# Performance work log

Measured on AMD Instinct MI355X. Metric: run time of the kernel, lower is better.

## Reference

```python
import jax, jax.numpy as jnp
import numpy as np

NUM_LEAVES = 8192
N_LAMBDA = 2101  # wavelengths 400..2500 nm

# ---- exponential integral E1(x), x > 0 (Abramowitz & Stegun 5.1.53 / 5.1.56) ----
# Ei(-x) = -E1(x) for x > 0; forward only ever calls expi on -kall with kall >= 1e-4.
_A = jnp.array([-0.57721566, 0.99999193, -0.24991055, 0.05519968, -0.00976004, 0.00107857], dtype=jnp.float32)
_PN = jnp.array([1.0, 8.5733287401, 18.0590169730, 8.6347608925, 0.2677737343], dtype=jnp.float32)
_PD = jnp.array([1.0, 9.5733223454, 25.6329561486, 21.0996530827, 3.9584969228], dtype=jnp.float32)

def _poly(c, x):
    r = c[0]
    for ci in c[1:]:
        r = r * x + ci
    return r

def _e1(x):
    # x > 0 guaranteed (kall clamped to >= 1e-4)
    small = -jnp.log(x) + _poly(_A[::-1], x)          # 0 < x <= 1
    big = jnp.exp(-x) / x * (_poly(_PN, x) / _poly(_PD, x))  # x > 1
    return jnp.where(x <= 1.0, small, big)

# ---- transmissivity of a dielectric plane (Stern / Allen) ----
def _getav(alpha_deg, nr):
    n2 = nr ** 2
    npx = n2 + 1.0
    nm = n2 - 1.0
    a = (nr + 1.0) * (nr + 1.0) / 2.0
    k = -(n2 - 1.0) * (n2 - 1.0) / 4.0
    rd = alpha_deg * (np.pi / 180.0)
    sa2 = np.sin(rd) ** 2  # python scalar
    if alpha_deg != 90.0:
        b1 = jnp.sqrt((sa2 - npx / 2.0) ** 2 + k)
    else:
        b1 = 0.0
    b2 = sa2 - npx / 2.0
    b = b1 - b2
    k2 = k ** 2
    ts = k2 / (6.0 * b ** 3) + k / b - b / 2.0 - (k2 / (6.0 * a ** 3) + k / a - a / 2.0)
    tp1 = -2.0 * n2 * (b - a) / npx ** 2
    nm2 = nm ** 2
    tp2 = -2.0 * n2 * npx * jnp.log(b / a) / nm2
    tp3 = n2 * (1.0 / b - 1.0 / a) / 2.0
    n22 = n2 ** 2
    npx3 = npx ** 3
    npax_a = 2.0 * npx * a - nm2
    npx_b = 2.0 * npx * b - nm2
    tp4 = 16.0 * n22 * (n22 + 1.0) * jnp.log(npx_b / npax_a) / (npx3 * nm2)
    tp5 = 16.0 * n2 ** 3 * (1.0 / npx_b - 1.0 / npax_a) / npx3
    tp = tp1 + tp2 + tp3 + tp4 + tp5
    return (ts + tp) / (2.0 * sa2)

def _forward(N, cab, car, water, lma, cant, nr, kab, kcar, kant, kw, km):
    # kall: [L, W] via broadcasting of [L,1] traits against [W] spectra
    kall = (cab * kab + car * kcar + cant * kant + water * kw + lma * km) / N
    kall = jnp.maximum(kall, 1e-4)
    # tau = (1-k)e^{-k} + k^2 * (-Ei(-k)) = (1-k)e^{-k} + k^2 E1(k)
    tau = (1.0 - kall) * jnp.exp(-kall) + kall ** 2 * _e1(kall)

    # one-layer reflectance/transmittance
    talf = _getav(40.0, nr)
    ralf = 1.0 - talf
    t12 = _getav(90.0, nr)
    r12 = 1.0 - t12
    t21 = t12 / (nr * nr)
    r21 = 1.0 - t21
    denom = 1.0 - r21 * r21 * tau * tau
    Ta = talf * tau * t21 / denom
    Ra = ralf + r21 * tau * Ta
    t = t12 * tau * t21 / denom
    r = r12 + r21 * tau * t

    rpt = r + t
    rmt = r - t
    mask = rpt >= 1.0  # [L, W]
    Dsq = (1.0 + rpt) * (1.0 + rmt) * (1.0 - rmt) * (1.0 - rpt)
    D = jnp.sqrt(jnp.where(mask, 1.0, Dsq))
    rqmtq = r ** 2 - t ** 2
    a = (1.0 + rqmtq + D) / (2.0 * r)
    b = (1.0 - rqmtq + D) / (2.0 * t)
    b_safe = jnp.where(mask, 1.0, b)  # guard pow with float exponent
    bnm1 = b_safe ** (N - 1.0)
    bn2 = bnm1 ** 2
    a2 = a * a
    den2 = a2 * bn2 - 1.0
    Rsub = a * (bn2 - 1.0) / den2
    Tsub = bnm1 * (a2 - 1.0) / den2
    # thick-layer (r+t >= 1) limit
    Tsub_alt = t / (t + (1.0 - t) * (N - 1.0))
    Tsub = jnp.where(mask, Tsub_alt, Tsub)
    Rsub = jnp.where(mask, 1.0 - Tsub_alt, Rsub)

    den3 = 1.0 - Rsub * r
    tran = Ta * Tsub / den3
    refl = Ra + Ta_Rsub_term(Ta, Rsub, t, den3)
    return refl, tran

def Ta_Rsub_term(Ta, Rsub, t, den3):
    return Ta * Rsub * t / den3

def setup_inputs() -> dict:
    key = jax.random.key(0)
    ks = jax.random.split(key, 12)
    u = lambda k, shp: jax.random.uniform(k, shp, dtype=jnp.float32)
    L, W = NUM_LEAVES, N_LAMBDA
    return {
        "N":     1.0 + 1.5 * u(ks[0], (L, 1)),      # leaf structure 1..2.5
        "cab":   10.0 + 70.0 * u(ks[1], (L, 1)),    # chlorophyll ug/cm2
        "car":   2.0 + 18.0 * u(ks[2], (L, 1)),     # carotenoids
        "water": 0.002 + 0.03 * u(ks[3], (L, 1)),   # EWT cm
        "lma":   0.005 + 0.03 * u(ks[4], (L, 1)),   # dry matter g/cm2
        "cant":  2.0 * u(ks[5], (L, 1)),            # anthocyanins
        "nr":    1.3 + 0.3 * u(ks[6], (W,)),        # refractive index
        "kab":   0.05 * u(ks[7], (W,)),
        "kcar":  0.05 * u(ks[8], (W,)),
        "kant":  0.05 * u(ks[9], (W,)),
        "kw":    30.0 * u(ks[10], (W,)),
        "km":    60.0 * u(ks[11], (W,)),
    }

def reference(N, cab, car, water, lma, cant, nr, kab, kcar, kant, kw, km):
    return _forward(N, cab, car, water, lma, cant, nr, kab, kcar, kant, kw, km)
```

## Files before the change

kernel.cpp:

```cpp
#include <hip/hip_runtime.h>

#define L_LEAVES 8192
#define W_LAMBDA 2101
#define WPAD     2104
#define SA2_40   0.41317591116653485f
#define LOG2E_F  1.4426950408889634f
#define LN2_F    0.6931471805599453f

__device__ __forceinline__ float rcpf(float x)  { return __builtin_amdgcn_rcpf(x); }
__device__ __forceinline__ float log2f_fast(float x) { return __builtin_amdgcn_logf(x); }
__device__ __forceinline__ float exp2f_fast(float x) { return __builtin_amdgcn_exp2f(x); }
__device__ __forceinline__ float sqrtf_fast(float x) { return __builtin_amdgcn_sqrtf(x); }

__device__ __forceinline__ float getav_dev(float sa2, bool is90, float nr) {
    float n2  = nr * nr;
    float npx = n2 + 1.0f;
    float nm  = n2 - 1.0f;
    float a   = (nr + 1.0f) * (nr + 1.0f) * 0.5f;
    float k   = -(n2 - 1.0f) * (n2 - 1.0f) * 0.25f;
    float b2  = sa2 - npx * 0.5f;
    float b1  = is90 ? 0.0f : sqrtf(b2 * b2 + k);
    float b   = b1 - b2;
    float k2  = k * k;
    float b3  = b * b * b;
    float a3  = a * a * a;
    float ts  = k2 / (6.0f * b3) + k / b - b * 0.5f
              - (k2 / (6.0f * a3) + k / a - a * 0.5f);
    float tp1 = -2.0f * n2 * (b - a) / (npx * npx);
    float nm2 = nm * nm;
    float tp2 = -2.0f * n2 * npx * logf(b / a) / nm2;
    float tp3 = n2 * (1.0f / b - 1.0f / a) * 0.5f;
    float n22 = n2 * n2;
    float npx3 = npx * npx * npx;
    float npax_a = 2.0f * npx * a - nm2;
    float npx_b  = 2.0f * npx * b - nm2;
    float tp4 = 16.0f * n22 * (n22 + 1.0f) * logf(npx_b / npax_a) / (npx3 * nm2);
    float tp5 = 16.0f * n2 * n2 * n2 * (1.0f / npx_b - 1.0f / npax_a) / npx3;
    float tp  = tp1 + tp2 + tp3 + tp4 + tp5;
    return (ts + tp) / (2.0f * sa2);
}

__global__ void precompute_kernel(const float* __restrict__ nr, float* __restrict__ tab) {
    int w = blockIdx.x * blockDim.x + threadIdx.x;
    if (w >= W_LAMBDA) return;
    float n    = nr[w];
    float talf = getav_dev(SA2_40, false, n);
    float t12  = getav_dev(1.0f,   true,  n);
    float t21  = t12 * rcpf(n * n);
    float r21  = 1.0f - t21;
    tab[0 * WPAD + w] = talf * t21;
    tab[1 * WPAD + w] = 1.0f - talf;
    tab[2 * WPAD + w] = t12 * t21;
    tab[3 * WPAD + w] = 1.0f - t12;
    tab[4 * WPAD + w] = r21;
    tab[5 * WPAD + w] = r21 * r21;
}

struct f4u { float v[4]; };

__device__ __forceinline__ float vget(const float4& v, int j) {
    return j == 0 ? v.x : (j == 1 ? v.y : (j == 2 ? v.z : v.w));
}

template<bool USE_TAB>
__global__ __launch_bounds__(192) void prospect_kernel(
    const float* __restrict__ pN,   const float* __restrict__ pcab,
    const float* __restrict__ pcar, const float* __restrict__ pwater,
    const float* __restrict__ plma, const float* __restrict__ pcant,
    const float* __restrict__ pnr,
    const float* __restrict__ pkab, const float* __restrict__ pkcar,
    const float* __restrict__ pkant, const float* __restrict__ pkw,
    const float* __restrict__ pkm,
    const float* __restrict__ tab,
    float* __restrict__ out)
{
    const int q  = blockIdx.x * blockDim.x + threadIdx.x;
    const int w0 = q * 4;
    if (w0 >= W_LAMBDA) return;
    const bool full = (w0 + 4 <= W_LAMBDA);

    const int l = blockIdx.y;
    const float Nl   = pN[l];
    const float invN = rcpf(Nl);
    const float Nm1  = Nl - 1.0f;
    const float cabl = pcab[l], carl = pcar[l], cantl = pcant[l];
    const float watl = pwater[l], lmal = plma[l];
    const size_t LW = (size_t)L_LEAVES * W_LAMBDA;

    float4 vkab, vkcar, vkant, vkw, vkm;
    float4 t0, t1, t2, t3, t4, t5;
    if (full) {
        vkab  = *(const float4*)(pkab  + w0);
        vkcar = *(const float4*)(pkcar + w0);
        vkant = *(const float4*)(pkant + w0);
        vkw   = *(const float4*)(pkw   + w0);
        vkm   = *(const float4*)(pkm   + w0);
        if (USE_TAB) {
            t0 = *(const float4*)(tab + 0 * WPAD + w0);
            t1 = *(const float4*)(tab + 1 * WPAD + w0);
            t2 = *(const float4*)(tab + 2 * WPAD + w0);
            t3 = *(const float4*)(tab + 3 * WPAD + w0);
            t4 = *(const float4*)(tab + 4 * WPAD + w0);
            t5 = *(const float4*)(tab + 5 * WPAD + w0);
        }
    } else {
        float* a[5] = {nullptr};
        #pragma unroll
        for (int j = 0; j < 4; ++j) {
            int w = min(w0 + j, W_LAMBDA - 1);
            ((float*)&vkab)[j]  = pkab[w];
            ((float*)&vkcar)[j] = pkcar[w];
            ((float*)&vkant)[j] = pkant[w];
            ((float*)&vkw)[j]   = pkw[w];
            ((float*)&vkm)[j]   = pkm[w];
            if (USE_TAB) {
                ((float*)&t0)[j] = tab[0 * WPAD + w];
                ((float*)&t1)[j] = tab[1 * WPAD + w];
                ((float*)&t2)[j] = tab[2 * WPAD + w];
                ((float*)&t3)[j] = tab[3 * WPAD + w];
                ((float*)&t4)[j] = tab[4 * WPAD + w];
                ((float*)&t5)[j] = tab[5 * WPAD + w];
            }
        }
        (void)a;
    }

    float rf[4], tr[4];
    #pragma unroll
    for (int j = 0; j < 4; ++j) {
        float c0, c1, c2, c3, c4, c5;
        if (USE_TAB) {
            c0 = vget(t0, j); c1 = vget(t1, j); c2 = vget(t2, j);
            c3 = vget(t3, j); c4 = vget(t4, j); c5 = vget(t5, j);
        } else {
            int w = min(w0 + j, W_LAMBDA - 1);
            float n    = pnr[w];
            float talf = getav_dev(SA2_40, false, n);
            float t12  = getav_dev(1.0f,   true,  n);
            float t21  = t12 * rcpf(n * n);
            float r21  = 1.0f - t21;
            c0 = talf * t21; c1 = 1.0f - talf; c2 = t12 * t21;
            c3 = 1.0f - t12; c4 = r21;         c5 = r21 * r21;
        }

        float k = (cabl * vget(vkab, j) + carl * vget(vkcar, j) + cantl * vget(vkant, j)
                 + watl * vget(vkw, j) + lmal * vget(vkm, j)) * invN;
        k = fmaxf(k, 1e-4f);

        float ek   = exp2f_fast(-k * LOG2E_F);
        float lg2k = log2f_fast(k);
        float poly = fmaf(fmaf(fmaf(fmaf(fmaf(0.00107857f, k, -0.00976004f), k, 0.05519968f),
                        k, -0.24991055f), k, 0.99999193f), k, -0.57721566f);
        float e1s  = fmaf(-LN2_F, lg2k, poly);
        float taus = fmaf(k * k, e1s, (1.0f - k) * ek);
        float pn = fmaf(fmaf(fmaf(fmaf(1.0f, k, 8.5733287401f), k, 18.0590169730f),
                       k, 8.6347608925f), k, 0.2677737343f);
        float pd = fmaf(fmaf(fmaf(fmaf(1.0f, k, 9.5733223454f), k, 25.6329561486f),
                       k, 21.0996530827f), k, 3.9584969228f);
        float taub = ek * fmaf(k, pn - pd, pd) * rcpf(pd);
        float tau  = (k <= 1.0f) ? taus : taub;

        float tau2 = tau * tau;
        float rd   = rcpf(fmaf(-c5, tau2, 1.0f));
        float Ta   = c0 * tau * rd;
        float tt   = c2 * tau * rd;
        float r21t = c4 * tau;
        float Ra   = fmaf(r21t, Ta, c1);
        float rr   = fmaf(r21t, tt, c3);

        float rpt  = rr + tt;
        float rmt  = rr - tt;
        bool  mask = (rpt >= 1.0f);
        float Dsq  = fmaf(-rmt, rmt, 1.0f) * fmaf(-rpt, rpt, 1.0f);
        float D    = sqrtf_fast(mask ? 1.0f : Dsq);
        float rq   = rpt * rmt;
        float s1   = 1.0f + D;
        float aa   = (s1 + rq) * rcpf(rr + rr);
        float bb   = (s1 - rq) * rcpf(tt + tt);
        float bsafe = mask ? 1.0f : bb;
        float bnm1 = exp2f_fast(Nm1 * log2f_fast(bsafe));
        float bn2  = bnm1 * bnm1;
        float a2   = aa * aa;
        float rdn  = rcpf(fmaf(a2, bn2, -1.0f));
        float Rsub = aa * (bn2 - 1.0f) * rdn;
        float Tsub = bnm1 * (a2 - 1.0f) * rdn;
        float Talt = tt * rcpf(fmaf(Nm1, 1.0f - tt, tt));
        if (mask) { Tsub = Talt; Rsub = 1.0f - Talt; }

        float r3   = rcpf(fmaf(-Rsub, rr, 1.0f));
        float g    = Ta * r3;
        tr[j] = g * Tsub;
        rf[j] = fmaf(g * Rsub, tt, Ra);
    }

    const size_t base = (size_t)l * W_LAMBDA + w0;
    if (full) {
        f4u fr; f4u ft;
        #pragma unroll
        for (int j = 0; j < 4; ++j) { fr.v[j] = rf[j]; ft.v[j] = tr[j]; }
        *reinterpret_cast<f4u*>(out + base)      = fr;
        *reinterpret_cast<f4u*>(out + LW + base) = ft;
    } else {
        out[base]      = rf[0];
        out[LW + base] = tr[0];
    }
}

extern "C" void kernel_launch(void* const* d_in, const int* in_sizes, int n_in,
                              void* d_out, int out_size, void* d_ws, size_t ws_size,
                              hipStream_t stream) {
    const float* pN     = (const float*)d_in[0];
    const float* pcab   = (const float*)d_in[1];
    const float* pcar   = (const float*)d_in[2];
    const float* pwater = (const float*)d_in[3];
    const float* plma   = (const float*)d_in[4];
    const float* pcant  = (const float*)d_in[5];
    const float* pnr    = (const float*)d_in[6];
    const float* pkab   = (const float*)d_in[7];
    const float* pkcar  = (const float*)d_in[8];
    const float* pkant  = (const float*)d_in[9];
    const float* pkw    = (const float*)d_in[10];
    const float* pkm    = (const float*)d_in[11];
    float* out = (float*)d_out;

    const int nquads = (W_LAMBDA + 3) / 4;
    dim3 grid((nquads + 191) / 192, L_LEAVES);
    dim3 block(192);

    const size_t tab_bytes = 6 * WPAD * sizeof(float);
    if (ws_size >= tab_bytes) {
        float* tabp = (float*)d_ws;
        precompute_kernel<<<(W_LAMBDA + 255) / 256, 256, 0, stream>>>(pnr, tabp);
        prospect_kernel<true><<<grid, block, 0, stream>>>(
            pN, pcab, pcar, pwater, plma, pcant, pnr,
            pkab, pkcar, pkant, pkw, pkm, (const float*)tabp, out);
    } else {
        prospect_kernel<false><<<grid, block, 0, stream>>>(
            pN, pcab, pcar, pwater, plma, pcant, pnr,
            pkab, pkcar, pkant, pkw, pkm, nullptr, out);
    }
}
```

Baseline: 61.22 us.

## Process eight leaves per thread to reuse per-wavelength spectra and table loads

Each thread now loops over eight leaves, loading the five absorption spectra and six Fresnel-table vectors once and reusing them across leaves instead of reloading per leaf. Block size drops to 64 threads and the grid's leaf dimension shrinks by eight, which cuts per-block overhead but also cuts the number of waves available to hide latency. Two reciprocals in the aa/bb computation are merged into one, and the Talt fallback now runs only when some lane in the wave takes it. The serial leaf loop raises per-thread work and may hurt overlap of stores with compute.

```diff
diff --git a/kernel.cpp b/kernel.cpp
--- a/kernel.cpp
+++ b/kernel.cpp
@@ -3,6 +3,7 @@
 #define L_LEAVES 8192
 #define W_LAMBDA 2101
 #define WPAD     2104
+#define NL       8
 #define SA2_40   0.41317591116653485f
 #define LOG2E_F  1.4426950408889634f
 #define LN2_F    0.6931471805599453f
@@ -63,7 +64,7 @@
 }
 
 template<bool USE_TAB>
-__global__ __launch_bounds__(192) void prospect_kernel(
+__global__ __launch_bounds__(64) void prospect_kernel(
     const float* __restrict__ pN,   const float* __restrict__ pcab,
     const float* __restrict__ pcar, const float* __restrict__ pwater,
     const float* __restrict__ plma, const float* __restrict__ pcant,
@@ -74,17 +75,11 @@
     const float* __restrict__ tab,
     float* __restrict__ out)
 {
-    const int q  = blockIdx.x * blockDim.x + threadIdx.x;
+    const int q  = blockIdx.x * 64 + threadIdx.x;
     const int w0 = q * 4;
     if (w0 >= W_LAMBDA) return;
     const bool full = (w0 + 4 <= W_LAMBDA);
-
-    const int l = blockIdx.y;
-    const float Nl   = pN[l];
-    const float invN = rcpf(Nl);
-    const float Nm1  = Nl - 1.0f;
-    const float cabl = pcab[l], carl = pcar[l], cantl = pcant[l];
-    const float watl = pwater[l], lmal = plma[l];
+    const int l0 = blockIdx.y * NL;
     const size_t LW = (size_t)L_LEAVES * W_LAMBDA;
 
     float4 vkab, vkcar, vkant, vkw, vkm;
@@ -95,16 +90,7 @@
         vkant = *(const float4*)(pkant + w0);
         vkw   = *(const float4*)(pkw   + w0);
         vkm   = *(const float4*)(pkm   + w0);
-        if (USE_TAB) {
-            t0 = *(const float4*)(tab + 0 * WPAD + w0);
-            t1 = *(const float4*)(tab + 1 * WPAD + w0);
-            t2 = *(const float4*)(tab + 2 * WPAD + w0);
-            t3 = *(const float4*)(tab + 3 * WPAD + w0);
-            t4 = *(const float4*)(tab + 4 * WPAD + w0);
-            t5 = *(const float4*)(tab + 5 * WPAD + w0);
-        }
     } else {
-        float* a[5] = {nullptr};
         #pragma unroll
         for (int j = 0; j < 4; ++j) {
             int w = min(w0 + j, W_LAMBDA - 1);
@@ -113,7 +99,20 @@
             ((float*)&vkant)[j] = pkant[w];
             ((float*)&vkw)[j]   = pkw[w];
             ((float*)&vkm)[j]   = pkm[w];
-            if (USE_TAB) {
+        }
+    }
+    if (USE_TAB) {
+        if (full) {
+            t0 = *(const float4*)(tab + 0 * WPAD + w0);
+            t1 = *(const float4*)(tab + 1 * WPAD + w0);
+            t2 = *(const float4*)(tab + 2 * WPAD + w0);
+            t3 = *(const float4*)(tab + 3 * WPAD + w0);
+            t4 = *(const float4*)(tab + 4 * WPAD + w0);
+            t5 = *(const float4*)(tab + 5 * WPAD + w0);
+        } else {
+            #pragma unroll
+            for (int j = 0; j < 4; ++j) {
+                int w = min(w0 + j, W_LAMBDA - 1);
                 ((float*)&t0)[j] = tab[0 * WPAD + w];
                 ((float*)&t1)[j] = tab[1 * WPAD + w];
                 ((float*)&t2)[j] = tab[2 * WPAD + w];
@@ -122,87 +121,103 @@
                 ((float*)&t5)[j] = tab[5 * WPAD + w];
             }
         }
-        (void)a;
-    }
-
-    float rf[4], tr[4];
-    #pragma unroll
-    for (int j = 0; j < 4; ++j) {
-        float c0, c1, c2, c3, c4, c5;
-        if (USE_TAB) {
-            c0 = vget(t0, j); c1 = vget(t1, j); c2 = vget(t2, j);
-            c3 = vget(t3, j); c4 = vget(t4, j); c5 = vget(t5, j);
-        } else {
+    } else {
+        #pragma unroll
+        for (int j = 0; j < 4; ++j) {
             int w = min(w0 + j, W_LAMBDA - 1);
             float n    = pnr[w];
             float talf = getav_dev(SA2_40, false, n);
             float t12  = getav_dev(1.0f,   true,  n);
             float t21  = t12 * rcpf(n * n);
             float r21  = 1.0f - t21;
-            c0 = talf * t21; c1 = 1.0f - talf; c2 = t12 * t21;
-            c3 = 1.0f - t12; c4 = r21;         c5 = r21 * r21;
-        }
-
-        float k = (cabl * vget(vkab, j) + carl * vget(vkcar, j) + cantl * vget(vkant, j)
-                 + watl * vget(vkw, j) + lmal * vget(vkm, j)) * invN;
-        k = fmaxf(k, 1e-4f);
-
-        float ek   = exp2f_fast(-k * LOG2E_F);
-        float lg2k = log2f_fast(k);
-        float poly = fmaf(fmaf(fmaf(fmaf(fmaf(0.00107857f, k, -0.00976004f), k, 0.05519968f),
-                        k, -0.24991055f), k, 0.99999193f), k, -0.57721566f);
-        float e1s  = fmaf(-LN2_F, lg2k, poly);
-        float taus = fmaf(k * k, e1s, (1.0f - k) * ek);
-        float pn = fmaf(fmaf(fmaf(fmaf(1.0f, k, 8.5733287401f), k, 18.0590169730f),
-                       k, 8.6347608925f), k, 0.2677737343f);
-        float pd = fmaf(fmaf(fmaf(fmaf(1.0f, k, 9.5733223454f), k, 25.6329561486f),
-                       k, 21.0996530827f), k, 3.9584969228f);
-        float taub = ek * fmaf(k, pn - pd, pd) * rcpf(pd);
-        float tau  = (k <= 1.0f) ? taus : taub;
-
-        float tau2 = tau * tau;
-        float rd   = rcpf(fmaf(-c5, tau2, 1.0f));
-        float Ta   = c0 * tau * rd;
-        float tt   = c2 * tau * rd;
-        float r21t = c4 * tau;
-        float Ra   = fmaf(r21t, Ta, c1);
-        float rr   = fmaf(r21t, tt, c3);
-
-        float rpt  = rr + tt;
-        float rmt  = rr - tt;
-        bool  mask = (rpt >= 1.0f);
-        float Dsq  = fmaf(-rmt, rmt, 1.0f) * fmaf(-rpt, rpt, 1.0f);
-        float D    = sqrtf_fast(mask ? 1.0f : Dsq);
-        float rq   = rpt * rmt;
-        float s1   = 1.0f + D;
-        float aa   = (s1 + rq) * rcpf(rr + rr);
-        float bb   = (s1 - rq) * rcpf(tt + tt);
-        float bsafe = mask ? 1.0f : bb;
-        float bnm1 = exp2f_fast(Nm1 * log2f_fast(bsafe));
-        float bn2  = bnm1 * bnm1;
-        float a2   = aa * aa;
-        float rdn  = rcpf(fmaf(a2, bn2, -1.0f));
-        float Rsub = aa * (bn2 - 1.0f) * rdn;
-        float Tsub = bnm1 * (a2 - 1.0f) * rdn;
-        float Talt = tt * rcpf(fmaf(Nm1, 1.0f - tt, tt));
-        if (mask) { Tsub = Talt; Rsub = 1.0f - Talt; }
-
-        float r3   = rcpf(fmaf(-Rsub, rr, 1.0f));
-        float g    = Ta * r3;
-        tr[j] = g * Tsub;
-        rf[j] = fmaf(g * Rsub, tt, Ra);
-    }
-
-    const size_t base = (size_t)l * W_LAMBDA + w0;
-    if (full) {
-        f4u fr; f4u ft;
+            ((float*)&t0)[j] = talf * t21;
+            ((float*)&t1)[j] = 1.0f - talf;
+            ((float*)&t2)[j] = t12 * t21;
+            ((float*)&t3)[j] = 1.0f - t12;
+            ((float*)&t4)[j] = r21;
+            ((float*)&t5)[j] = r21 * r21;
+        }
+    }
+
+    #pragma unroll 1
+    for (int il = 0; il < NL; ++il) {
+        const int l = l0 + il;
+        const float Nl   = pN[l];
+        const float invN = rcpf(Nl);
+        const float Nm1  = Nl - 1.0f;
+        const float cabl = pcab[l], carl = pcar[l], cantl = pcant[l];
+        const float watl = pwater[l], lmal = plma[l];
+
+        float rf[4], tr[4];
         #pragma unroll
-        for (int j = 0; j < 4; ++j) { fr.v[j] = rf[j]; ft.v[j] = tr[j]; }
-        *reinterpret_cast<f4u*>(out + base)      = fr;
-        *reinterpret_cast<f4u*>(out + LW + base) = ft;
-    } else {
-        out[base]      = rf[0];
-        out[LW + base] = tr[0];
+        for (int j = 0; j < 4; ++j) {
+            const float c0 = vget(t0, j), c1 = vget(t1, j), c2 = vget(t2, j);
+            const float c3 = vget(t3, j), c4 = vget(t4, j), c5 = vget(t5, j);
+
+            float k = (cabl * vget(vkab, j) + carl * vget(vkcar, j) + cantl * vget(vkant, j)
+                     + watl * vget(vkw, j) + lmal * vget(vkm, j)) * invN;
+            k = fmaxf(k, 1e-4f);
+
+            float ek   = exp2f_fast(-k * LOG2E_F);
+            float lg2k = log2f_fast(k);
+            float poly = fmaf(fmaf(fmaf(fmaf(fmaf(0.00107857f, k, -0.00976004f), k, 0.05519968f),
+                            k, -0.24991055f), k, 0.99999193f), k, -0.57721566f);
+            float e1s  = fmaf(-LN2_F, lg2k, poly);
+            float taus = fmaf(k * k, e1s, (1.0f - k) * ek);
+            float pn = fmaf(fmaf(fmaf(fmaf(1.0f, k, 8.5733287401f), k, 18.0590169730f),
+                           k, 8.6347608925f), k, 0.2677737343f);
+            float pd = fmaf(fmaf(fmaf(fmaf(1.0f, k, 9.5733223454f), k, 25.6329561486f),
+                           k, 21.0996530827f), k, 3.9584969228f);
+            float taub = ek * fmaf(k, pn - pd, pd) * rcpf(pd);
+            float tau  = (k <= 1.0f) ? taus : taub;
+
+            float tau2 = tau * tau;
+            float rd   = rcpf(fmaf(-c5, tau2, 1.0f));
+            float Ta   = c0 * tau * rd;
+            float tt   = c2 * tau * rd;
+            float r21t = c4 * tau;
+            float Ra   = fmaf(r21t, Ta, c1);
+            float rr   = fmaf(r21t, tt, c3);
+
+            float rpt  = rr + tt;
+            float rmt  = rr - tt;
+            bool  mask = (rpt >= 1.0f);
+            float Dsq  = fmaf(-rmt, rmt, 1.0f) * fmaf(-rpt, rpt, 1.0f);
+            float D    = sqrtf_fast(mask ? 1.0f : Dsq);
+            float rq   = rpt * rmt;
+            float s1   = 1.0f + D;
+            float rp2  = rcpf((rr * tt) * 4.0f);
+            float aa   = (s1 + rq) * (rp2 * (tt + tt));
+            float bb   = (s1 - rq) * (rp2 * (rr + rr));
+            float bsafe = mask ? 1.0f : bb;
+            float bnm1 = exp2f_fast(Nm1 * log2f_fast(bsafe));
+            float bn2  = bnm1 * bnm1;
+            float a2   = aa * aa;
+            float rdn  = rcpf(fmaf(a2, bn2, -1.0f));
+            float Rsub = aa * (bn2 - 1.0f) * rdn;
+            float Tsub = bnm1 * (a2 - 1.0f) * rdn;
+            if (__any((int)mask)) {
+                float Talt = tt * rcpf(fmaf(Nm1, 1.0f - tt, tt));
+                if (mask) { Tsub = Talt; Rsub = 1.0f - Talt; }
+            }
+
+            float r3   = rcpf(fmaf(-Rsub, rr, 1.0f));
+            float g    = Ta * r3;
+            tr[j] = g * Tsub;
+            rf[j] = fmaf(g * Rsub, tt, Ra);
+        }
+
+        const size_t base = (size_t)l * W_LAMBDA + w0;
+        if (full) {
+            f4u fr; f4u ft;
+            #pragma unroll
+            for (int j = 0; j < 4; ++j) { fr.v[j] = rf[j]; ft.v[j] = tr[j]; }
+            *reinterpret_cast<f4u*>(out + base)      = fr;
+            *reinterpret_cast<f4u*>(out + LW + base) = ft;
+        } else {
+            out[base]      = rf[0];
+            out[LW + base] = tr[0];
+        }
     }
 }
 
@@ -224,8 +239,8 @@
     float* out = (float*)d_out;
 
     const int nquads = (W_LAMBDA + 3) / 4;
-    dim3 grid((nquads + 191) / 192, L_LEAVES);
-    dim3 block(192);
+    dim3 grid((nquads + 63) / 64, L_LEAVES / NL);
+    dim3 block(64);
 
     const size_t tab_bytes = 6 * WPAD * sizeof(float);
     if (ws_size >= tab_bytes) {
```

Result: slower. 64.09 us (+4.7%).
